# Kernel tuning notes

Measured on AMD Instinct MI355X. Metric: run time of the kernel, lower is better.

## Reference

```python
import jax, jax.numpy as jnp
import numpy as np

N_NODES = 100000
N_EDGES = 1600000
C_IN = 500
HIDDEN = 256
C_OUT = 50
K = 10
K_HALF = K // 2  # 5
ALPHA = 0.1


def _prop(x, src, dst, norm, n):
    # one propagate(): gather source features, scale by edge norm, scatter-add to dst
    msg = norm[:, None] * x[src]          # [E, F]
    return jax.ops.segment_sum(msg, dst, num_segments=n)


def setup_inputs() -> dict:
    key = jax.random.key(0)
    k0, k1, k2, k3 = jax.random.split(key, 4)
    x = jax.random.normal(k0, (N_NODES, C_IN), dtype=jnp.float32)
    edge_index = jax.random.randint(k1, (2, N_EDGES), 0, N_NODES, dtype=jnp.int32)
    # temp[k] = alpha * (1-alpha)^(2k), k = 0..K//2  (even-order PPR coefficients)
    temp = jnp.asarray(ALPHA * (1.0 - ALPHA) ** (2 * np.arange(K_HALF + 1)), dtype=jnp.float32)
    W1 = jax.random.normal(k2, (C_IN, HIDDEN), dtype=jnp.float32) / np.sqrt(C_IN).astype(np.float32)
    b1 = jnp.zeros((HIDDEN,), jnp.float32)
    W2 = jax.random.normal(k3, (HIDDEN, C_OUT), dtype=jnp.float32) / np.sqrt(HIDDEN).astype(np.float32)
    b2 = jnp.zeros((C_OUT,), jnp.float32)
    return {"x": x, "edge_index": edge_index, "W1": W1, "b1": b1, "W2": W2, "b2": b2, "temp": temp}


def reference(x, edge_index, W1, b1, W2, b2, temp):
    n = x.shape[0]
    src, dst = edge_index[0], edge_index[1]
    # sym-normalized adjacency A_hat = D^-1/2 A D^-1/2.
    # (get_laplacian 'sym' then add_self_loops(-norm, 1.0): the -1/+1 diagonal
    #  entries cancel under scatter-add, leaving exactly A_hat.)
    deg = jax.ops.segment_sum(jnp.ones_like(src, dtype=x.dtype), src, num_segments=n)
    dinv = jnp.where(deg > 0, jax.lax.rsqrt(jnp.maximum(deg, 1e-12)), 0.0)
    norm = dinv[src] * dinv[dst]          # [E]

    # MLP (dropout is identity in eval mode)
    h = jax.nn.relu(x @ W1 + b1)
    h = h @ W2 + b2                        # [N, C_OUT]

    hidden0 = h * temp[0]

    def body(k, carry):
        xk, hid = carry
        xk = _prop(xk, src, dst, norm, n)  # A_hat @ x
        xk = _prop(xk, src, dst, norm, n)  # A_hat^2 @ x
        hid = hid + temp[k + 1] * xk
        return (xk, hid)

    _, hidden = jax.lax.fori_loop(0, K_HALF, body, (h, hidden0))
    return jax.nn.log_softmax(hidden, axis=1)
```

## Files before the change

### kernel.cpp

```cpp
#include <hip/hip_runtime.h>

#define NN 100000
#define CIN 500
#define KPAD 512
#define HID 256
#define COUT 50
#define NPADOUT 64
#define FPAD 64

#define NBLK 256
#define CB 128
#define NC ((NN + CB - 1) / CB)
#define NCB (NC * NBLK)
#define NCB2 (2 * NCB)

typedef __attribute__((ext_vector_type(8))) short short8;
typedef __attribute__((ext_vector_type(4))) float f32x4;

static __device__ __forceinline__ unsigned short f2bf(float f) {
  union { float f; unsigned u; } v; v.f = f;
  unsigned r = (v.u + 0x7fffu + ((v.u >> 16) & 1u)) >> 16;
  return (unsigned short)r;
}

static __device__ __forceinline__ int slotAt(const int* __restrict__ incl,
                                             const int* __restrict__ bpre, int g) {
  return g ? incl[g - 1] + bpre[(g - 1) >> 10] : 0;
}


__launch_bounds__(256)
__global__ void k_p1(const int* __restrict__ src, const int* __restrict__ dst,
                     int* __restrict__ blk_cnt, int E, int chunk) {
  __shared__ int bd[NC], bs[NC];
  int tid = threadIdx.x;
  for (int i = tid; i < NC; i += 256) { bd[i] = 0; bs[i] = 0; }
  __syncthreads();
  int e0 = blockIdx.x * chunk, e1 = min(E, e0 + chunk);
  for (int e = e0 + tid; e < e1; e += 256) {
    atomicAdd(&bd[dst[e] >> 7], 1);
    atomicAdd(&bs[src[e] >> 7], 1);
  }
  __syncthreads();
  for (int i = tid; i < NC; i += 256) {
    blk_cnt[i * NBLK + blockIdx.x] = bd[i];
    blk_cnt[NCB + i * NBLK + blockIdx.x] = bs[i];
  }
}


__global__ void k_scan_a(const int* __restrict__ hist, int* __restrict__ incl,
                         int* __restrict__ bsum, int n) {
  __shared__ int ts[256];
  int tid = threadIdx.x;
  int base = blockIdx.x * 1024 + tid * 4;
  int a0 = 0, a1 = 0, a2 = 0, a3 = 0;
  if (base + 3 < n) {
    a0 = hist[base]; a1 = hist[base + 1]; a2 = hist[base + 2]; a3 = hist[base + 3];
  } else {
    if (base     < n) a0 = hist[base];
    if (base + 1 < n) a1 = hist[base + 1];
    if (base + 2 < n) a2 = hist[base + 2];
    if (base + 3 < n) a3 = hist[base + 3];
  }
  a1 += a0; a2 += a1; a3 += a2;
  ts[tid] = a3;
  __syncthreads();
  for (int o = 1; o < 256; o <<= 1) {
    int v = ts[tid];
    if (tid >= o) v += ts[tid - o];
    __syncthreads();
    ts[tid] = v;
    __syncthreads();
  }
  int ex = tid ? ts[tid - 1] : 0;
  if (base     < n) incl[base]     = a0 + ex;
  if (base + 1 < n) incl[base + 1] = a1 + ex;
  if (base + 2 < n) incl[base + 2] = a2 + ex;
  if (base + 3 < n) incl[base + 3] = a3 + ex;
  if (tid == 255) bsum[blockIdx.x] = ts[255];
}

__global__ void k_scan_b(const int* __restrict__ bsum, int* __restrict__ bpre, int nb) {
  __shared__ int s[512];
  int tid = threadIdx.x;
  s[tid] = (tid < nb) ? bsum[tid] : 0;
  __syncthreads();
  for (int o = 1; o < 512; o <<= 1) {
    int v = s[tid];
    if (tid >= o) v += s[tid - o];
    __syncthreads();
    s[tid] = v;
    __syncthreads();
  }
  if (tid < nb) bpre[tid] = tid ? s[tid - 1] : 0;
}


__launch_bounds__(256)
__global__ void k_p2(const int* __restrict__ src, const int* __restrict__ dst,
                     const int* __restrict__ incl, const int* __restrict__ bpre,
                     int* __restrict__ pkd, unsigned char* __restrict__ pks, int E, int chunk) {
  __shared__ int cd[NC], cs[NC];
  int tid = threadIdx.x;
  for (int i = tid; i < NC; i += 256) {
    cd[i] = slotAt(incl, bpre, i * NBLK + blockIdx.x);
    cs[i] = slotAt(incl, bpre, NCB + i * NBLK + blockIdx.x) - E;
  }
  __syncthreads();
  int e0 = blockIdx.x * chunk, e1 = min(E, e0 + chunk);
  for (int e = e0 + tid; e < e1; e += 256) {
    int s = src[e], d = dst[e];
    int pd = atomicAdd(&cd[d >> 7], 1);
    pkd[pd] = (s << 7) | (d & 127);
    int ps = atomicAdd(&cs[s >> 7], 1);
    pks[ps] = (unsigned char)(s & 127);
  }
}


__launch_bounds__(256)
__global__ void k_p3s(const int* __restrict__ incl, const int* __restrict__ bpre,
                      const unsigned char* __restrict__ pks, float* __restrict__ dinv, int E) {
  __shared__ int hist[CB];
  int b = blockIdx.x, tid = threadIdx.x;
  if (tid < CB) hist[tid] = 0;
  __syncthreads();
  int s0 = slotAt(incl, bpre, NCB + b * NBLK) - E;
  int s1 = slotAt(incl, bpre, NCB + (b + 1) * NBLK) - E;
  for (int e = s0 + tid; e < s1; e += 256) atomicAdd(&hist[pks[e]], 1);
  __syncthreads();
  if (tid < CB) {
    int node = b * CB + tid;
    if (node < NN) {
      int c = hist[tid];
      dinv[node] = c > 0 ? rsqrtf((float)c) : 0.f;
    }
  }
}


__launch_bounds__(256)
__global__ void k_p3d(const int* __restrict__ incl, const int* __restrict__ bpre,
                      const int* __restrict__ pkd, const float* __restrict__ dinv,
                      int* __restrict__ offs, int2* __restrict__ epk, int E) {
  __shared__ int hist[CB], base[CB], cur[CB];
  int b = blockIdx.x, tid = threadIdx.x;
  if (tid < CB) hist[tid] = 0;
  __syncthreads();
  int s0 = slotAt(incl, bpre, b * NBLK);
  int s1 = slotAt(incl, bpre, (b + 1) * NBLK);
  for (int e = s0 + tid; e < s1; e += 256) atomicAdd(&hist[pkd[e] & 127], 1);
  __syncthreads();
  if (tid == 0) {
    int acc = s0;
    for (int i = 0; i < CB; i++) { base[i] = acc; cur[i] = acc; acc += hist[i]; }
  }
  __syncthreads();
  if (tid < CB) {
    int node = b * CB + tid;
    if (node < NN) offs[node] = base[tid];
  }
  if (b == gridDim.x - 1 && tid == 0) offs[NN] = E;
  for (int e = s0 + tid; e < s1; e += 256) {
    int pk = pkd[e];
    int fine = pk & 127, s = pk >> 7;
    int pos = atomicAdd(&cur[fine], 1);
    float nm = dinv[s] * dinv[b * CB + fine];
    epk[pos] = make_int2(s, __float_as_int(nm));
  }
}


__global__ void k_wt(const float* __restrict__ W1, const float* __restrict__ W2,
                     unsigned short* __restrict__ W1T, unsigned short* __restrict__ W2T) {
  int idx = blockIdx.x * 256 + threadIdx.x;
  if (idx < HID * KPAD) {
    int n = idx >> 9, k = idx & 511;
    W1T[idx] = (k < CIN) ? f2bf(W1[(long)k * HID + n]) : (unsigned short)0;
  } else if (idx < HID * KPAD + NPADOUT * HID) {
    int i2 = idx - HID * KPAD;
    int n = i2 >> 8, k = i2 & 255;
    W2T[i2] = (n < COUT) ? f2bf(W2[(long)k * COUT + n]) : (unsigned short)0;
  }
}


#define LOADS(ra0_, ra1_, rb0_, rb1_, kkc)                                        \
  {                                                                               \
    const int kk_ = (kkc);                                                        \
    bool okk = kk_ + sc * 4 <= 496;                                               \
    if (okA && okk) ra0_ = *reinterpret_cast<const float4*>(&X[xbaseA + kk_]);    \
    else { ra0_.x = ra0_.y = ra0_.z = ra0_.w = 0.f; }                             \
    if (okB && okk) ra1_ = *reinterpret_cast<const float4*>(&X[xbaseB + kk_]);    \
    else { ra1_.x = ra1_.y = ra1_.z = ra1_.w = 0.f; }                             \
    rb0_ = *reinterpret_cast<const uint4*>(&W1T[wbase0 + kk_]);                   \
    rb1_ = *reinterpret_cast<const uint4*>(&W1T[wbase1 + kk_]);                   \
  }

#define STORE_LDS(As_, Bs_, ra0_, ra1_, rb0_, rb1_)                               \
  {                                                                               \
    ushort4 v0, v1;                                                               \
    v0.x = f2bf(ra0_.x); v0.y = f2bf(ra0_.y); v0.z = f2bf(ra0_.z); v0.w = f2bf(ra0_.w); \
    v1.x = f2bf(ra1_.x); v1.y = f2bf(ra1_.y); v1.z = f2bf(ra1_.z); v1.w = f2bf(ra1_.w); \
    *reinterpret_cast<ushort4*>(&As_[sr * 40 + sc * 4]) = v0;                     \
    *reinterpret_cast<ushort4*>(&As_[(sr + 64) * 40 + sc * 4]) = v1;              \
    *reinterpret_cast<uint4*>(&Bs_[br * 40 + bc * 8]) = rb0_;                     \
    *reinterpret_cast<uint4*>(&Bs_[(br + 128) * 40 + bc * 8]) = rb1_;             \
  }

#define COMPUTE(As_, Bs_)                                                         \
  {                                                                               \
    short8 af[4], bfr[4];                                                         \
    const int koff = (lane >> 4) * 8;                                             \
    _Pragma("unroll")                                                             \
    for (int i = 0; i < 4; i++)                                                   \
      af[i] = *reinterpret_cast<const short8*>(&As_[(wr * 64 + i * 16 + (lane & 15)) * 40 + koff]); \
    _Pragma("unroll")                                                             \
    for (int j = 0; j < 4; j++)                                                   \
      bfr[j] = *reinterpret_cast<const short8*>(&Bs_[(wc * 64 + j * 16 + (lane & 15)) * 40 + koff]); \
    _Pragma("unroll")                                                             \
    for (int i = 0; i < 4; i++)                                                   \
      _Pragma("unroll")                                                           \
      for (int j = 0; j < 4; j++)                                                 \
        acc[i][j] = __builtin_amdgcn_mfma_f32_16x16x32_bf16(af[i], bfr[j], acc[i][j], 0, 0, 0); \
  }

__launch_bounds__(512)
__global__ void k_mlp(const float* __restrict__ X, const unsigned short* __restrict__ W1T,
                      const float* __restrict__ b1, const unsigned short* __restrict__ W2T,
                      const float* __restrict__ b2, const float* __restrict__ temp,
                      unsigned short* __restrict__ X0B, float* __restrict__ HIDB) {
  __shared__ unsigned short smem[2 * 15360];
  const int tid = threadIdx.x;
  const int lane = tid & 63, w = tid >> 6;
  const int wr = w >> 2, wc = w & 3;
  const int row0 = blockIdx.x * 128;
  f32x4 acc[4][4] = {};
  const int sr = tid >> 3, sc = tid & 7;
  const int br = tid >> 2, bc = tid & 3;

  float4 raA0, raA1; uint4 rbA0, rbA1;
  float4 raB0, raB1; uint4 rbB0, rbB1;

  const int growA = row0 + sr;
  const int growB = row0 + sr + 64;
  const bool okA = growA < NN, okB = growB < NN;
  const long xbaseA = (long)growA * CIN + sc * 4;
  const long xbaseB = (long)growB * CIN + sc * 4;
  const long wbase0 = (long)br * KPAD + bc * 8;
  const long wbase1 = (long)(br + 128) * KPAD + bc * 8;

  LOADS(raA0, raA1, rbA0, rbA1, 0);
  LOADS(raB0, raB1, rbB0, rbB1, 32);

#pragma unroll
  for (int tt = 0; tt < 8; tt++) {
    const int kk0 = tt * 64;
    {
      unsigned short* As = smem;
      unsigned short* Bs = smem + 128 * 40;
      STORE_LDS(As, Bs, raA0, raA1, rbA0, rbA1);
      __syncthreads();
      if (kk0 + 64 < KPAD) LOADS(raA0, raA1, rbA0, rbA1, kk0 + 64);
      COMPUTE(As, Bs);
    }
    {
      unsigned short* As = smem + 15360;
      unsigned short* Bs = As + 128 * 40;
      STORE_LDS(As, Bs, raB0, raB1, rbB0, rbB1);
      __syncthreads();
      if (kk0 + 96 < KPAD) LOADS(raB0, raB1, rbB0, rbB1, kk0 + 96);
      COMPUTE(As, Bs);
    }
  }

  unsigned short* Hs = smem;
  const float t0 = temp[0];
  const int rt = w >> 1;
  const int jh = w & 1;
#pragma unroll
  for (int ph = 0; ph < 2; ph++) {
    __syncthreads();
    if (wr == ph) {
#pragma unroll
      for (int i = 0; i < 4; i++) {
        int lr = i * 16 + (lane >> 4) * 4;
#pragma unroll
        for (int j = 0; j < 4; j++) {
          int col = wc * 64 + j * 16 + (lane & 15);
          float bv = b1[col];
#pragma unroll
          for (int r = 0; r < 4; r++) {
            float v = acc[i][j][r] + bv;
            v = v > 0.f ? v : 0.f;
            Hs[(lr + r) * 264 + col] = f2bf(v);
          }
        }
      }
    }
    __syncthreads();
    f32x4 acc2[2] = {};
    const int koff = (lane >> 4) * 8;
    for (int kk = 0; kk < HID; kk += 32) {
      short8 a = *reinterpret_cast<const short8*>(&Hs[(rt * 16 + (lane & 15)) * 264 + kk + koff]);
#pragma unroll
      for (int jj = 0; jj < 2; jj++) {
        int n = (jh * 2 + jj) * 16 + (lane & 15);
        short8 b = *reinterpret_cast<const short8*>(&W2T[n * HID + kk + koff]);
        acc2[jj] = __builtin_amdgcn_mfma_f32_16x16x32_bf16(a, b, acc2[jj], 0, 0, 0);
      }
    }
#pragma unroll
    for (int jj = 0; jj < 2; jj++) {
      int col = (jh * 2 + jj) * 16 + (lane & 15);
      float bv = (col < COUT) ? b2[col] : 0.f;
#pragma unroll
      for (int r = 0; r < 4; r++) {
        int row = row0 + ph * 64 + rt * 16 + (lane >> 4) * 4 + r;
        if (row < NN) {
          float v = acc2[jj][r] + bv;
          X0B[((long)row << 6) + col] = f2bf(v);
          if (col < COUT) HIDB[(long)row * COUT + col] = t0 * v;
        }
      }
    }
  }
}


__launch_bounds__(256)
__global__ void k_prop(const int* __restrict__ offs, const int2* __restrict__ epk,
                       const unsigned short* __restrict__ xin,
                       unsigned short* __restrict__ xout, float* __restrict__ hid,
                       const float* __restrict__ temp, int accidx) {
  int node = blockIdx.x * 16 + (threadIdx.x >> 4);
  if (node >= NN) return;
  int h = threadIdx.x & 15;
  int fp = h * 4;
  int s0 = offs[node], s1 = offs[node + 1];
  float a0 = 0.f, a1 = 0.f, a2 = 0.f, a3 = 0.f;
  int e = s0;
  for (; e + 7 < s1; e += 8) {
    int2 p[8];
#pragma unroll
    for (int q = 0; q < 8; q++) p[q] = epk[e + q];
    uint2 v[8];
#pragma unroll
    for (int q = 0; q < 8; q++)
      v[q] = *reinterpret_cast<const uint2*>(&xin[((long)p[q].x << 6) + fp]);
#pragma unroll
    for (int q = 0; q < 8; q++) {
      float wq = __int_as_float(p[q].y);
      a0 += wq * __uint_as_float(v[q].x << 16);
      a1 += wq * __uint_as_float(v[q].x & 0xffff0000u);
      a2 += wq * __uint_as_float(v[q].y << 16);
      a3 += wq * __uint_as_float(v[q].y & 0xffff0000u);
    }
  }
  for (; e + 3 < s1; e += 4) {
    int2 p0 = epk[e], p1 = epk[e + 1], p2 = epk[e + 2], p3 = epk[e + 3];
    uint2 v0 = *reinterpret_cast<const uint2*>(&xin[((long)p0.x << 6) + fp]);
    uint2 v1 = *reinterpret_cast<const uint2*>(&xin[((long)p1.x << 6) + fp]);
    uint2 v2 = *reinterpret_cast<const uint2*>(&xin[((long)p2.x << 6) + fp]);
    uint2 v3 = *reinterpret_cast<const uint2*>(&xin[((long)p3.x << 6) + fp]);
    float w0 = __int_as_float(p0.y), w1 = __int_as_float(p1.y);
    float w2 = __int_as_float(p2.y), w3 = __int_as_float(p3.y);
    a0 += w0 * __uint_as_float(v0.x << 16) + w1 * __uint_as_float(v1.x << 16)
        + w2 * __uint_as_float(v2.x << 16) + w3 * __uint_as_float(v3.x << 16);
    a1 += w0 * __uint_as_float(v0.x & 0xffff0000u) + w1 * __uint_as_float(v1.x & 0xffff0000u)
        + w2 * __uint_as_float(v2.x & 0xffff0000u) + w3 * __uint_as_float(v3.x & 0xffff0000u);
    a2 += w0 * __uint_as_float(v0.y << 16) + w1 * __uint_as_float(v1.y << 16)
        + w2 * __uint_as_float(v2.y << 16) + w3 * __uint_as_float(v3.y << 16);
    a3 += w0 * __uint_as_float(v0.y & 0xffff0000u) + w1 * __uint_as_float(v1.y & 0xffff0000u)
        + w2 * __uint_as_float(v2.y & 0xffff0000u) + w3 * __uint_as_float(v3.y & 0xffff0000u);
  }
  for (; e < s1; e++) {
    int2 p0 = epk[e];
    float w0 = __int_as_float(p0.y);
    uint2 v0 = *reinterpret_cast<const uint2*>(&xin[((long)p0.x << 6) + fp]);
    a0 += w0 * __uint_as_float(v0.x << 16);
    a1 += w0 * __uint_as_float(v0.x & 0xffff0000u);
    a2 += w0 * __uint_as_float(v0.y << 16);
    a3 += w0 * __uint_as_float(v0.y & 0xffff0000u);
  }
  unsigned d0 = ((unsigned)f2bf(a1) << 16) | (unsigned)f2bf(a0);
  unsigned d1 = ((unsigned)f2bf(a3) << 16) | (unsigned)f2bf(a2);
  if (h <= 11) {
    uint2 pk2; pk2.x = d0; pk2.y = d1;
    *reinterpret_cast<uint2*>(&xout[((long)node << 6) + fp]) = pk2;
  } else if (h == 12) {
    *reinterpret_cast<unsigned*>(&xout[((long)node << 6) + fp]) = d0;
  }
  if (accidx >= 0) {
    float t = temp[accidx];
    if (h <= 11) {
      float2* hp0 = reinterpret_cast<float2*>(&hid[(long)node * COUT + fp]);
      float2 o0 = *hp0;
      o0.x += t * a0; o0.y += t * a1;
      *hp0 = o0;
      float2* hp1 = reinterpret_cast<float2*>(&hid[(long)node * COUT + fp + 2]);
      float2 o1 = *hp1;
      o1.x += t * a2; o1.y += t * a3;
      *hp1 = o1;
    } else if (h == 12) {
      float2* hp0 = reinterpret_cast<float2*>(&hid[(long)node * COUT + fp]);
      float2 o0 = *hp0;
      o0.x += t * a0; o0.y += t * a1;
      *hp0 = o0;
    }
  }
}


__launch_bounds__(256)
__global__ void k_lsm(const float* __restrict__ hid, float* __restrict__ out) {
  int node = blockIdx.x * 4 + (threadIdx.x >> 6);
  if (node >= NN) return;
  int f = threadIdx.x & 63;
  float v = (f < COUT) ? hid[(long)node * COUT + f] : -INFINITY;
  float m = v;
#pragma unroll
  for (int o = 32; o > 0; o >>= 1) m = fmaxf(m, __shfl_xor(m, o, 64));
  float ex = (f < COUT) ? expf(v - m) : 0.f;
  float s = ex;
#pragma unroll
  for (int o = 32; o > 0; o >>= 1) s += __shfl_xor(s, o, 64);
  if (f < COUT) out[(long)node * COUT + f] = (v - m) - logf(s);
}


extern "C" void kernel_launch(void* const* d_in, const int* in_sizes, int n_in,
                              void* d_out, int out_size, void* d_ws, size_t ws_size,
                              hipStream_t stream) {
  const float* X  = (const float*)d_in[0];
  const int* EI   = (const int*)d_in[1];
  const float* W1 = (const float*)d_in[2];
  const float* B1 = (const float*)d_in[3];
  const float* W2 = (const float*)d_in[4];
  const float* B2 = (const float*)d_in[5];
  const float* TEMP = (const float*)d_in[6];
  const int E = in_sizes[1] / 2;
  const int* src = EI;
  const int* dst = EI + E;

  char* ws = (char*)d_ws;
  size_t off = 0;
  auto alloc = [&](size_t bytes) -> void* {
    off = (off + 511) & ~(size_t)511;
    void* p = ws + off;
    off += bytes;
    return p;
  };
  unsigned short* W1T = (unsigned short*)alloc((size_t)HID * KPAD * 2);
  unsigned short* W2T = (unsigned short*)alloc((size_t)NPADOUT * HID * 2);
  unsigned short* X0B = (unsigned short*)alloc((size_t)NN * FPAD * 2);
  unsigned short* X1B = (unsigned short*)alloc((size_t)NN * FPAD * 2);
  float* HIDB = (float*)alloc((size_t)NN * COUT * 4);
  float* DINV = (float*)alloc((size_t)NN * 4);
  int* OFFS   = (int*)alloc((size_t)(NN + 1) * 4);
  int* BLKC   = (int*)alloc((size_t)NCB2 * 4);
  int* INCL   = (int*)alloc((size_t)NCB2 * 4);
  int* BSUM   = (int*)alloc(512 * 4);
  int* BPRE   = (int*)alloc(512 * 4);
  int* PKD    = (int*)alloc((size_t)E * 4);
  unsigned char* PKS = (unsigned char*)alloc((size_t)E);
  int2* EPK   = (int2*)alloc((size_t)E * 8);

  const int chunk = (E + NBLK - 1) / NBLK;
  const int nsa = (NCB2 + 1023) / 1024;

  k_p1<<<NBLK, 256, 0, stream>>>(src, dst, BLKC, E, chunk);
  k_scan_a<<<nsa, 256, 0, stream>>>(BLKC, INCL, BSUM, NCB2);
  k_scan_b<<<1, 512, 0, stream>>>(BSUM, BPRE, nsa);
  k_p2<<<NBLK, 256, 0, stream>>>(src, dst, INCL, BPRE, PKD, PKS, E, chunk);
  k_p3s<<<NC, 256, 0, stream>>>(INCL, BPRE, PKS, DINV, E);
  k_p3d<<<NC, 256, 0, stream>>>(INCL, BPRE, PKD, DINV, OFFS, EPK, E);

  k_wt<<<(HID * KPAD + NPADOUT * HID + 255) / 256, 256, 0, stream>>>(W1, W2, W1T, W2T);

  k_mlp<<<(NN + 127) / 128, 512, 0, stream>>>(X, W1T, B1, W2T, B2, TEMP, X0B, HIDB);

  const int PB = (NN + 15) / 16;
  for (int k = 0; k < 5; k++) {
    k_prop<<<PB, 256, 0, stream>>>(OFFS, EPK, X0B, X1B, HIDB, TEMP, -1);
    k_prop<<<PB, 256, 0, stream>>>(OFFS, EPK, X1B, X0B, HIDB, TEMP, k + 1);
  }
  k_lsm<<<(NN + 3) / 4, 256, 0, stream>>>(HIDB, (float*)d_out);
}
```

Measured before the change: 825.7 us.

## Defer hidden accumulation to final kernel and use nontemporal edge loads/stores

Removes the fp32 hidden-state read-modify-write from every second propagation kernel and from the MLP epilogue. Each even-order propagation result is now kept in its own bf16 buffer, and a fused final kernel forms the weighted sum and log-softmax. Edge-list loads and output stores are also marked nontemporal to reduce cache pollution during the random feature gathers. In exchange it uses more workspace and sums the hidden terms from bf16-rounded values instead of fp32 accumulators. The nontemporal store on xout may also push data out of cache that the next propagation reads straight away.

```diff
diff --git a/kernel.cpp b/kernel.cpp
--- a/kernel.cpp
+++ b/kernel.cpp
@@ -229,8 +229,7 @@
 __launch_bounds__(512)
 __global__ void k_mlp(const float* __restrict__ X, const unsigned short* __restrict__ W1T,
                       const float* __restrict__ b1, const unsigned short* __restrict__ W2T,
-                      const float* __restrict__ b2, const float* __restrict__ temp,
-                      unsigned short* __restrict__ X0B, float* __restrict__ HIDB) {
+                      const float* __restrict__ b2, unsigned short* __restrict__ X0B) {
   __shared__ unsigned short smem[2 * 15360];
   const int tid = threadIdx.x;
   const int lane = tid & 63, w = tid >> 6;
@@ -276,7 +275,6 @@
   }
 
   unsigned short* Hs = smem;
-  const float t0 = temp[0];
   const int rt = w >> 1;
   const int jh = w & 1;
 #pragma unroll
@@ -321,7 +319,6 @@
         if (row < NN) {
           float v = acc2[jj][r] + bv;
           X0B[((long)row << 6) + col] = f2bf(v);
-          if (col < COUT) HIDB[(long)row * COUT + col] = t0 * v;
         }
       }
     }
@@ -332,8 +329,8 @@
 __launch_bounds__(256)
 __global__ void k_prop(const int* __restrict__ offs, const int2* __restrict__ epk,
                        const unsigned short* __restrict__ xin,
-                       unsigned short* __restrict__ xout, float* __restrict__ hid,
-                       const float* __restrict__ temp, int accidx) {
+                       unsigned short* __restrict__ xout) {
+  const long long* __restrict__ epk8 = reinterpret_cast<const long long*>(epk);
   int node = blockIdx.x * 16 + (threadIdx.x >> 4);
   if (node >= NN) return;
   int h = threadIdx.x & 15;
@@ -342,16 +339,16 @@
   float a0 = 0.f, a1 = 0.f, a2 = 0.f, a3 = 0.f;
   int e = s0;
   for (; e + 7 < s1; e += 8) {
-    int2 p[8];
-#pragma unroll
-    for (int q = 0; q < 8; q++) p[q] = epk[e + q];
+    long long p[8];
+#pragma unroll
+    for (int q = 0; q < 8; q++) p[q] = __builtin_nontemporal_load(&epk8[e + q]);
     uint2 v[8];
 #pragma unroll
     for (int q = 0; q < 8; q++)
-      v[q] = *reinterpret_cast<const uint2*>(&xin[((long)p[q].x << 6) + fp]);
+      v[q] = *reinterpret_cast<const uint2*>(&xin[((long)(int)p[q] << 6) + fp]);
 #pragma unroll
     for (int q = 0; q < 8; q++) {
-      float wq = __int_as_float(p[q].y);
+      float wq = __int_as_float((int)(p[q] >> 32));
       a0 += wq * __uint_as_float(v[q].x << 16);
       a1 += wq * __uint_as_float(v[q].x & 0xffff0000u);
       a2 += wq * __uint_as_float(v[q].y << 16);
@@ -359,13 +356,16 @@
     }
   }
   for (; e + 3 < s1; e += 4) {
-    int2 p0 = epk[e], p1 = epk[e + 1], p2 = epk[e + 2], p3 = epk[e + 3];
-    uint2 v0 = *reinterpret_cast<const uint2*>(&xin[((long)p0.x << 6) + fp]);
-    uint2 v1 = *reinterpret_cast<const uint2*>(&xin[((long)p1.x << 6) + fp]);
-    uint2 v2 = *reinterpret_cast<const uint2*>(&xin[((long)p2.x << 6) + fp]);
-    uint2 v3 = *reinterpret_cast<const uint2*>(&xin[((long)p3.x << 6) + fp]);
-    float w0 = __int_as_float(p0.y), w1 = __int_as_float(p1.y);
-    float w2 = __int_as_float(p2.y), w3 = __int_as_float(p3.y);
+    long long p0 = __builtin_nontemporal_load(&epk8[e]);
+    long long p1 = __builtin_nontemporal_load(&epk8[e + 1]);
+    long long p2 = __builtin_nontemporal_load(&epk8[e + 2]);
+    long long p3 = __builtin_nontemporal_load(&epk8[e + 3]);
+    uint2 v0 = *reinterpret_cast<const uint2*>(&xin[((long)(int)p0 << 6) + fp]);
+    uint2 v1 = *reinterpret_cast<const uint2*>(&xin[((long)(int)p1 << 6) + fp]);
+    uint2 v2 = *reinterpret_cast<const uint2*>(&xin[((long)(int)p2 << 6) + fp]);
+    uint2 v3 = *reinterpret_cast<const uint2*>(&xin[((long)(int)p3 << 6) + fp]);
+    float w0 = __int_as_float((int)(p0 >> 32)), w1 = __int_as_float((int)(p1 >> 32));
+    float w2 = __int_as_float((int)(p2 >> 32)), w3 = __int_as_float((int)(p3 >> 32));
     a0 += w0 * __uint_as_float(v0.x << 16) + w1 * __uint_as_float(v1.x << 16)
         + w2 * __uint_as_float(v2.x << 16) + w3 * __uint_as_float(v3.x << 16);
     a1 += w0 * __uint_as_float(v0.x & 0xffff0000u) + w1 * __uint_as_float(v1.x & 0xffff0000u)
@@ -376,9 +376,9 @@
         + w2 * __uint_as_float(v2.y & 0xffff0000u) + w3 * __uint_as_float(v3.y & 0xffff0000u);
   }
   for (; e < s1; e++) {
-    int2 p0 = epk[e];
-    float w0 = __int_as_float(p0.y);
-    uint2 v0 = *reinterpret_cast<const uint2*>(&xin[((long)p0.x << 6) + fp]);
+    long long p0 = __builtin_nontemporal_load(&epk8[e]);
+    float w0 = __int_as_float((int)(p0 >> 32));
+    uint2 v0 = *reinterpret_cast<const uint2*>(&xin[((long)(int)p0 << 6) + fp]);
     a0 += w0 * __uint_as_float(v0.x << 16);
     a1 += w0 * __uint_as_float(v0.x & 0xffff0000u);
     a2 += w0 * __uint_as_float(v0.y << 16);
@@ -387,38 +387,37 @@
   unsigned d0 = ((unsigned)f2bf(a1) << 16) | (unsigned)f2bf(a0);
   unsigned d1 = ((unsigned)f2bf(a3) << 16) | (unsigned)f2bf(a2);
   if (h <= 11) {
-    uint2 pk2; pk2.x = d0; pk2.y = d1;
-    *reinterpret_cast<uint2*>(&xout[((long)node << 6) + fp]) = pk2;
+    unsigned long long pk8 = ((unsigned long long)d1 << 32) | d0;
+    __builtin_nontemporal_store(pk8,
+        reinterpret_cast<unsigned long long*>(&xout[((long)node << 6) + fp]));
   } else if (h == 12) {
-    *reinterpret_cast<unsigned*>(&xout[((long)node << 6) + fp]) = d0;
-  }
-  if (accidx >= 0) {
-    float t = temp[accidx];
-    if (h <= 11) {
-      float2* hp0 = reinterpret_cast<float2*>(&hid[(long)node * COUT + fp]);
-      float2 o0 = *hp0;
-      o0.x += t * a0; o0.y += t * a1;
-      *hp0 = o0;
-      float2* hp1 = reinterpret_cast<float2*>(&hid[(long)node * COUT + fp + 2]);
-      float2 o1 = *hp1;
-      o1.x += t * a2; o1.y += t * a3;
-      *hp1 = o1;
-    } else if (h == 12) {
-      float2* hp0 = reinterpret_cast<float2*>(&hid[(long)node * COUT + fp]);
-      float2 o0 = *hp0;
-      o0.x += t * a0; o0.y += t * a1;
-      *hp0 = o0;
-    }
-  }
-}
-
-
-__launch_bounds__(256)
-__global__ void k_lsm(const float* __restrict__ hid, float* __restrict__ out) {
+    __builtin_nontemporal_store(d0,
+        reinterpret_cast<unsigned*>(&xout[((long)node << 6) + fp]));
+  }
+}
+
+
+__launch_bounds__(256)
+__global__ void k_fin(const unsigned short* __restrict__ x0,
+                      const unsigned short* __restrict__ x1,
+                      const unsigned short* __restrict__ x2,
+                      const unsigned short* __restrict__ x3,
+                      const unsigned short* __restrict__ x4,
+                      const unsigned short* __restrict__ x5,
+                      const float* __restrict__ temp, float* __restrict__ out) {
   int node = blockIdx.x * 4 + (threadIdx.x >> 6);
   if (node >= NN) return;
   int f = threadIdx.x & 63;
-  float v = (f < COUT) ? hid[(long)node * COUT + f] : -INFINITY;
+  float v = -INFINITY;
+  if (f < COUT) {
+    long idx = ((long)node << 6) + f;
+    v = temp[0] * __uint_as_float((unsigned)x0[idx] << 16)
+      + temp[1] * __uint_as_float((unsigned)x1[idx] << 16)
+      + temp[2] * __uint_as_float((unsigned)x2[idx] << 16)
+      + temp[3] * __uint_as_float((unsigned)x3[idx] << 16)
+      + temp[4] * __uint_as_float((unsigned)x4[idx] << 16)
+      + temp[5] * __uint_as_float((unsigned)x5[idx] << 16);
+  }
   float m = v;
 #pragma unroll
   for (int o = 32; o > 0; o >>= 1) m = fmaxf(m, __shfl_xor(m, o, 64));
@@ -454,9 +453,8 @@
   };
   unsigned short* W1T = (unsigned short*)alloc((size_t)HID * KPAD * 2);
   unsigned short* W2T = (unsigned short*)alloc((size_t)NPADOUT * HID * 2);
-  unsigned short* X0B = (unsigned short*)alloc((size_t)NN * FPAD * 2);
-  unsigned short* X1B = (unsigned short*)alloc((size_t)NN * FPAD * 2);
-  float* HIDB = (float*)alloc((size_t)NN * COUT * 4);
+  unsigned short* XB[7];
+  for (int i = 0; i < 7; i++) XB[i] = (unsigned short*)alloc((size_t)NN * FPAD * 2);
   float* DINV = (float*)alloc((size_t)NN * 4);
   int* OFFS   = (int*)alloc((size_t)(NN + 1) * 4);
   int* BLKC   = (int*)alloc((size_t)NCB2 * 4);
@@ -479,12 +477,13 @@
 
   k_wt<<<(HID * KPAD + NPADOUT * HID + 255) / 256, 256, 0, stream>>>(W1, W2, W1T, W2T);
 
-  k_mlp<<<(NN + 127) / 128, 512, 0, stream>>>(X, W1T, B1, W2T, B2, TEMP, X0B, HIDB);
+  k_mlp<<<(NN + 127) / 128, 512, 0, stream>>>(X, W1T, B1, W2T, B2, XB[0]);
 
   const int PB = (NN + 15) / 16;
   for (int k = 0; k < 5; k++) {
-    k_prop<<<PB, 256, 0, stream>>>(OFFS, EPK, X0B, X1B, HIDB, TEMP, -1);
-    k_prop<<<PB, 256, 0, stream>>>(OFFS, EPK, X1B, X0B, HIDB, TEMP, k + 1);
-  }
-  k_lsm<<<(NN + 3) / 4, 256, 0, stream>>>(HIDB, (float*)d_out);
-}
+    k_prop<<<PB, 256, 0, stream>>>(OFFS, EPK, XB[k], XB[6]);
+    k_prop<<<PB, 256, 0, stream>>>(OFFS, EPK, XB[6], XB[k + 1]);
+  }
+  k_fin<<<(NN + 3) / 4, 256, 0, stream>>>(XB[0], XB[1], XB[2], XB[3], XB[4], XB[5],
+                                          TEMP, (float*)d_out);
+}
```

Measured after the change: 907.9 us. 1.1x slower.
